# Kernel optimization log

Hardware: AMD Instinct MI355X
Metric: run time of the kernel (lower is better)

## Reference

```python
import jax, jax.numpy as jnp
import numpy as np

NUM_HEADS = 16
HEAD_DIM = 80
HIDDEN = 1280
SEQ = 3072
NUM_SEGS = 6  # 6 packed images of 512 patches each


def rotate_half(x):
    x1, x2 = jnp.split(x, 2, axis=-1)
    return jnp.concatenate([-x2, x1], axis=-1)


def setup_inputs() -> dict:
    key = jax.random.key(0)
    ks = jax.random.split(key, 6)
    hidden_states = jax.random.normal(ks[0], (SEQ, HIDDEN), dtype=jnp.float32)
    # RoPE tables as in Qwen-VL vision: freqs over half the head_dim, duplicated
    half = HEAD_DIM // 2
    inv_freq = 1.0 / (10000.0 ** (jnp.arange(half, dtype=jnp.float32) / half))
    pos = jnp.arange(SEQ, dtype=jnp.float32)[:, None]
    freqs = pos * inv_freq[None, :]                      # (SEQ, half)
    emb = jnp.concatenate([freqs, freqs], axis=-1)       # (SEQ, HEAD_DIM)
    cos = jnp.cos(emb)
    sin = jnp.sin(emb)
    # Packed segment boundaries: [0, 512, 1024, ..., 3072]
    cu_seqlens = jnp.arange(0, SEQ + 1, SEQ // NUM_SEGS, dtype=jnp.int32)
    scale = 0.02
    w_qkv = jax.random.normal(ks[1], (3 * HIDDEN, HIDDEN), dtype=jnp.float32) * scale
    b_qkv = jax.random.normal(ks[2], (3 * HIDDEN,), dtype=jnp.float32) * scale
    w_proj = jax.random.normal(ks[3], (HIDDEN, HIDDEN), dtype=jnp.float32) * scale
    b_proj = jax.random.normal(ks[4], (HIDDEN,), dtype=jnp.float32) * scale
    return {
        "hidden_states": hidden_states, "cos": cos, "sin": sin,
        "w_qkv": w_qkv, "b_qkv": b_qkv, "w_proj": w_proj, "b_proj": b_proj,
        "cu_seqlens": cu_seqlens,
    }


def reference(hidden_states, cos, sin, w_qkv, b_qkv, w_proj, b_proj, cu_seqlens):
    S, H = hidden_states.shape
    nh, hd = NUM_HEADS, H // NUM_HEADS

    # Fused QKV projection: (S, 3H) -> q, k, v each (S, nh, hd)
    qkv = hidden_states @ w_qkv.T + b_qkv
    qkv = qkv.reshape(S, 3, nh, hd)
    q, k, v = qkv[:, 0], qkv[:, 1], qkv[:, 2]

    # Inline RoPE on q/k (cos/sin broadcast over heads)
    c = cos[:, None, :]
    s = sin[:, None, :]
    q = q * c + rotate_half(q) * s
    k = k * c + rotate_half(k) * s

    # Original casts fp32 -> fp16 for the flash attention kernel
    q16 = q.astype(jnp.float16)
    k16 = k.astype(jnp.float16)
    v16 = v.astype(jnp.float16)

    # Varlen masking: tokens attend only within their own packed segment
    tok = jnp.arange(S)
    seg = jnp.searchsorted(cu_seqlens, tok, side="right")  # (S,)
    same_seg = seg[:, None] == seg[None, :]                 # (S, S)

    scale = hd ** (-0.5)
    # Scores accumulated in fp32 (as flash attention does internally)
    scores = jnp.einsum("qhd,khd->hqk", q16, k16,
                        preferred_element_type=jnp.float32) * scale
    scores = jnp.where(same_seg[None], scores, jnp.finfo(jnp.float32).min)
    weights = jax.nn.softmax(scores, axis=-1).astype(jnp.float16)  # (nh, S, S)

    attn = jnp.einsum("hqk,khd->qhd", weights, v16)  # (S, nh, hd) fp16
    attn = attn.astype(jnp.float32).reshape(S, H)
    return attn @ w_proj.T + b_proj
```

## Files before the change

### kernel.cpp

```cpp
#include <hip/hip_runtime.h>

typedef _Float16 f16;
typedef _Float16 half8 __attribute__((ext_vector_type(8)));
typedef _Float16 half4 __attribute__((ext_vector_type(4)));
typedef float f32x4 __attribute__((ext_vector_type(4)));

__device__ __forceinline__ void gld_lds16(const void* g, void* l) {
  __builtin_amdgcn_global_load_lds((const __attribute__((address_space(1))) void*)g,
                                   (__attribute__((address_space(3))) void*)l, 16, 0, 0);
}

template <int CTRL>
__device__ __forceinline__ float dppf(float x) {
  return __builtin_bit_cast(float,
      __builtin_amdgcn_mov_dpp(__builtin_bit_cast(int, x), CTRL, 0xf, 0xf, true));
}
__device__ __forceinline__ float dpp_max16(float v) {
  v = fmaxf(v, dppf<0xB1>(v));
  v = fmaxf(v, dppf<0x4E>(v));
  v = fmaxf(v, dppf<0x128>(v));
  v = fmaxf(v, dppf<0x140>(v));
  return v;
}
__device__ __forceinline__ float dpp_sum16(float v) {
  v += dppf<0xB1>(v);
  v += dppf<0x4E>(v);
  v += dppf<0x128>(v);
  v += dppf<0x140>(v);
  return v;
}

__global__ void cvt_all(const float* __restrict__ hid, const float* __restrict__ wq,
                        const float* __restrict__ wp, f16* __restrict__ hid16,
                        f16* __restrict__ wq16, f16* __restrict__ wp16) {
  int b = blockIdx.x;
  const float* in;
  f16* out;
  int i;
  if (b < 3840) { in = hid; out = hid16; i = b * 256 + threadIdx.x; }
  else if (b < 8640) { in = wq; out = wq16; i = (b - 3840) * 256 + threadIdx.x; }
  else { in = wp; out = wp16; i = (b - 8640) * 256 + threadIdx.x; }
  float4 v = ((const float4*)in)[i];
  half4 o;
  o.x = (f16)v.x; o.y = (f16)v.y; o.z = (f16)v.z; o.w = (f16)v.w;
  ((half4*)out)[i] = o;
}

__global__ __launch_bounds__(256, 2) void gemm240(const f16* __restrict__ A,
                                                  const f16* __restrict__ B,
                                                  const float* __restrict__ bias,
                                                  f16* __restrict__ C) {
  __shared__ f16 S[40960];
  char* Sb = (char*)S;
  const int tid = threadIdx.x, lane = tid & 63, wid = tid >> 6;
  const int lm = lane & 15, q4 = lane >> 4;
  const int wm = wid >> 1, wn = wid & 1;
  const int swz = ((int)blockIdx.x & 7) * 60 + ((int)blockIdx.x >> 3);
  const int bm = (swz % 24) * 128, bn = (swz / 24) * 192;

  const int ch = ((lane & 7) ^ (lane >> 3)) << 3;
  uint32_t aoff[4], boff[6];
#pragma unroll
  for (int j = 0; j < 4; j++)
    aoff[j] = (uint32_t)((bm + (j * 4 + wid) * 8 + (lane >> 3)) * 1280 + ch);
#pragma unroll
  for (int i = 0; i < 6; i++)
    boff[i] = (uint32_t)((bn + wid * 48 + i * 8 + (lane >> 3)) * 1280 + ch);

  const int xr = (lm & 7) << 4;
  int aro[4][2], bro[6][2];
#pragma unroll
  for (int f = 0; f < 4; f++)
#pragma unroll
    for (int ks = 0; ks < 2; ks++)
      aro[f][ks] = (wm * 64 + f * 16 + lm) * 128 + ((ks * 64 + q4 * 16) ^ xr);
#pragma unroll
  for (int n = 0; n < 6; n++)
#pragma unroll
    for (int ks = 0; ks < 2; ks++)
      bro[n][ks] = (wn * 96 + n * 16 + lm) * 128 + ((ks * 64 + q4 * 16) ^ xr);

  f32x4 acc[4][6] = {};

  {
#pragma unroll
    for (int j = 0; j < 4; j++)
      gld_lds16(A + aoff[j], Sb + (j * 4 + wid) * 1024);
#pragma unroll
    for (int i = 0; i < 6; i++)
      gld_lds16(B + boff[i], Sb + 32768 + (wid * 6 + i) * 1024);
    gld_lds16(A + aoff[0] + 64, Sb + 16384 + wid * 1024);
    gld_lds16(A + aoff[2] + 64, Sb + 16384 + (8 + wid) * 1024);
#pragma unroll
    for (int i = 0; i < 6; i++)
      gld_lds16(B + boff[i] + 64, Sb + 32768 + 24576 + (wid * 6 + i) * 1024);
    asm volatile("s_waitcnt vmcnt(8)" ::: "memory");
    __builtin_amdgcn_s_barrier();
  }

  constexpr int NT = 20;
  for (int t = 0; t < NT; ++t) {
    const int p = t & 1;
    char* Ab = Sb + p * 16384;
    char* Bb = Sb + 32768 + p * 24576;
    char* An = Sb + (p ^ 1) * 16384;
    const int k1 = (t + 1) * 64, k2 = (t + 2) * 64;

    half8 a0[2][2], bf[6][2];
#pragma unroll
    for (int f = 0; f < 2; f++)
#pragma unroll
      for (int ks = 0; ks < 2; ks++)
        a0[f][ks] = *(const half8*)(Ab + aro[f][ks]);
#pragma unroll
    for (int n = 0; n < 6; n++)
#pragma unroll
      for (int ks = 0; ks < 2; ks++)
        bf[n][ks] = *(const half8*)(Bb + bro[n][ks]);
    if (t + 1 < NT) {
      gld_lds16(A + aoff[1] + k1, An + (4 + wid) * 1024);
      gld_lds16(A + aoff[3] + k1, An + (12 + wid) * 1024);
    }
    __builtin_amdgcn_s_setprio(1);
#pragma unroll
    for (int ks = 0; ks < 2; ks++)
#pragma unroll
      for (int f = 0; f < 2; f++)
#pragma unroll
        for (int n = 0; n < 6; n++)
          acc[f][n] =
              __builtin_amdgcn_mfma_f32_16x16x32_f16(a0[f][ks], bf[n][ks], acc[f][n], 0, 0, 0);
    __builtin_amdgcn_s_setprio(0);
    __builtin_amdgcn_sched_barrier(0);
    asm volatile("s_waitcnt lgkmcnt(0)" ::: "memory");
    __builtin_amdgcn_s_barrier();

#pragma unroll
    for (int f = 0; f < 2; f++)
#pragma unroll
      for (int ks = 0; ks < 2; ks++)
        a0[f][ks] = *(const half8*)(Ab + aro[2 + f][ks]);
    if (t + 2 < NT) {
      gld_lds16(A + aoff[0] + k2, Ab + wid * 1024);
      gld_lds16(A + aoff[2] + k2, Ab + (8 + wid) * 1024);
#pragma unroll
      for (int i = 0; i < 6; i++)
        gld_lds16(B + boff[i] + k2, Bb + (wid * 6 + i) * 1024);
    }
    __builtin_amdgcn_s_setprio(1);
#pragma unroll
    for (int ks = 0; ks < 2; ks++)
#pragma unroll
      for (int f = 0; f < 2; f++)
#pragma unroll
        for (int n = 0; n < 6; n++)
          acc[2 + f][n] = __builtin_amdgcn_mfma_f32_16x16x32_f16(a0[f][ks], bf[n][ks],
                                                                 acc[2 + f][n], 0, 0, 0);
    __builtin_amdgcn_s_setprio(0);
    __builtin_amdgcn_sched_barrier(0);
    if (t + 2 < NT) {
      asm volatile("s_waitcnt vmcnt(8)" ::: "memory");
    } else {
      asm volatile("s_waitcnt vmcnt(0)" ::: "memory");
    }
    asm volatile("s_waitcnt lgkmcnt(0)" ::: "memory");
    __builtin_amdgcn_s_barrier();
  }

#pragma unroll
  for (int f = 0; f < 4; f++)
#pragma unroll
    for (int n = 0; n < 6; n++) {
      const int gc = bn + wn * 96 + n * 16 + lm;
      const float bb = bias[gc];
      const int gr0 = bm + wm * 64 + f * 16 + q4 * 4;
#pragma unroll
      for (int r = 0; r < 4; r++)
        C[(size_t)(gr0 + r) * 3840 + gc] = (f16)(acc[f][n][r] + bb);
    }
}

template <bool OUT_F16>
__global__ __launch_bounds__(256, 2) void gemm_bt64(const f16* __restrict__ A,
                                                    const f16* __restrict__ B,
                                                    const float* __restrict__ bias,
                                                    void* __restrict__ Cout,
                                                    int K, int lda, int ldb, int ldc) {
  __shared__ f16 As[64 * 32];
  __shared__ f16 Bs[128 * 32];
  const int tid = threadIdx.x, lane = tid & 63, wave = tid >> 6;
  const int bm = blockIdx.x * 64, bn = blockIdx.y * 128;
  const int wm = (wave & 1) * 32, wn = (wave >> 1) * 64;
  const int lm = lane & 15, kq = (lane >> 4) * 8;
  const int arow = tid >> 2, acol = (tid & 3) * 8;

  const f16* Ab = A + (size_t)(bm + arow) * lda + acol;
  const f16* Bb = B + (size_t)(bn + arow) * ldb + acol;
  f16* AsW = As + wave * 512;
  f16* BsW = Bs + wave * 512;

  f32x4 acc[2][4] = {};
  for (int k0 = 0; k0 < K; k0 += 32) {
    gld_lds16(Ab + k0, AsW);
    gld_lds16(Bb + k0, BsW);
    gld_lds16(Bb + (size_t)64 * ldb + k0, BsW + 2048);
    __syncthreads();
    half8 af[2], bf[4];
#pragma unroll
    for (int mt = 0; mt < 2; mt++) af[mt] = *(const half8*)&As[(wm + 16 * mt + lm) * 32 + kq];
#pragma unroll
    for (int nt = 0; nt < 4; nt++) bf[nt] = *(const half8*)&Bs[(wn + 16 * nt + lm) * 32 + kq];
#pragma unroll
    for (int mt = 0; mt < 2; mt++)
#pragma unroll
      for (int nt = 0; nt < 4; nt++)
        acc[mt][nt] = __builtin_amdgcn_mfma_f32_16x16x32_f16(af[mt], bf[nt], acc[mt][nt], 0, 0, 0);
    __syncthreads();
  }
  const int q4 = lane >> 4;
#pragma unroll
  for (int mt = 0; mt < 2; mt++)
#pragma unroll
    for (int nt = 0; nt < 4; nt++)
#pragma unroll
      for (int r = 0; r < 4; r++) {
        int gr = bm + wm + 16 * mt + 4 * q4 + r;
        int gc = bn + wn + 16 * nt + lm;
        float v = acc[mt][nt][r] + bias[gc];
        if (OUT_F16)
          ((f16*)Cout)[(size_t)gr * ldc + gc] = (f16)v;
        else
          ((float*)Cout)[(size_t)gr * ldc + gc] = v;
      }
}

__global__ void rope_transpose(f16* __restrict__ qkv, const float* __restrict__ cosb,
                               const float* __restrict__ sinb, f16* __restrict__ vt) {
  __shared__ f16 tile[64][72];
  const int b = blockIdx.x;
  if (b < 1920) {
    int idx = b * 256 + threadIdx.x;
    int c = idx % 5;
    int t = idx / 5;
    int h = t % 16; t /= 16;
    int qk = t & 1;
    int s = t >> 1;
    size_t base = (size_t)s * 3840 + qk * 1280 + h * 80 + c * 8;
    half8 x = *(half8*)&qkv[base];
    half8 y = *(half8*)&qkv[base + 40];
    const float* cp = cosb + s * 80 + c * 8;
    const float* sp = sinb + s * 80 + c * 8;
    half8 ox, oy;
#pragma unroll
    for (int i = 0; i < 8; i++) {
      float cs = cp[i], sn = sp[i];
      float xf = (float)x[i], yf = (float)y[i];
      ox[i] = (f16)(xf * cs - yf * sn);
      oy[i] = (f16)(yf * cs + xf * sn);
    }
    *(half8*)&qkv[base] = ox;
    *(half8*)&qkv[base + 40] = oy;
  } else {
    const int bb = b - 1920;
    const int bs = (bb % 48) * 64;
    const int bd = (bb / 48) * 64;
    const int r = threadIdx.x >> 2, c = (threadIdx.x & 3) * 16;
    *(uint4*)&tile[r][c] = *(const uint4*)&qkv[(size_t)(bs + r) * 3840 + 2560 + bd + c];
    *(uint4*)&tile[r][c + 8] = *(const uint4*)&qkv[(size_t)(bs + r) * 3840 + 2560 + bd + c + 8];
    __syncthreads();
    f16 tmp[16];
#pragma unroll
    for (int i = 0; i < 16; i++) tmp[i] = tile[c + i][r];
    *(uint4*)&vt[(size_t)(bd + r) * 3072 + bs + c] = *(uint4*)&tmp[0];
    *(uint4*)&vt[(size_t)(bd + r) * 3072 + bs + c + 8] = *(uint4*)&tmp[8];
  }
}

__global__ __launch_bounds__(256, 3) void flash_attn6(const f16* __restrict__ qkv,
                                                      const f16* __restrict__ vt,
                                                      f16* __restrict__ attn) {
  __shared__ f16 S[25088];
  const int tid = threadIdx.x, lane = tid & 63, wave = tid >> 6;
  const int lm = lane & 15, q4 = lane >> 4;
  const int h = blockIdx.x, g = blockIdx.z;
  const int qbase = g * 512 + blockIdx.y * 64 + wave * 16;
  f16* P = S + 20480 + wave * 1152;
  const half8 hz = {};

  const f16* qrow = qkv + (size_t)(qbase + lm) * 3840 + h * 80;
  half8 qf[3];
  qf[0] = *(const half8*)(qrow + q4 * 8);
  qf[1] = *(const half8*)(qrow + 32 + q4 * 8);
  qf[2] = (q4 < 2) ? *(const half8*)(qrow + 64 + q4 * 8) : hz;

  const bool isK = wave < 2;
  const f16* gsrc = isK ? qkv : vt;
  const uint32_t gstep = isK ? (uint32_t)(64 * 3840) : 64u;
  const int cbase = (wave & 1) * 5;
  const uint32_t ldsoff = (isK ? 0u : 5120u) + (uint32_t)cbase * 512u;
  uint32_t goff[5];
#pragma unroll
  for (int i = 0; i < 5; i++) {
    int t = (cbase + i) * 1024 + lane * 16;
    if (isK) {
      int row = t / 160, colb = t % 160;
      goff[i] = (uint32_t)((g * 512 + row) * 3840 + 1280 + h * 80 + (colb >> 1));
    } else {
      int vd = t >> 7, vsb = t & 127;
      int vsrc = vsb ^ ((vd & 7) << 4);
      goff[i] = (uint32_t)((h * 80 + vd) * 3072 + g * 512 + (vsrc >> 1));
    }
  }

  f32x4 oacc[5] = {};
  float mprev[4] = {-1e30f, -1e30f, -1e30f, -1e30f};
  float lsum[4] = {0.f, 0.f, 0.f, 0.f};
  const float sc = 0.11180339887498949f * 1.4426950408889634f;

#pragma unroll
  for (int i = 0; i < 5; i++) gld_lds16(gsrc + goff[i], S + ldsoff + i * 512);
  __syncthreads();

  for (int jj = 0; jj < 8; jj++) {
    const int p = jj & 1;
    f16* Kb = S + p * 10240;
    f16* Vb = Kb + 5120;
    if (jj < 7) {
#pragma unroll
      for (int i = 0; i < 5; i++)
        gld_lds16(gsrc + goff[i] + (uint32_t)(jj + 1) * gstep,
                  S + (p ^ 1) * 10240 + ldsoff + i * 512);
    }

    f32x4 sacc[4] = {};
#pragma unroll
    for (int ks = 0; ks < 3; ks++) {
      half8 bk[4];
#pragma unroll
      for (int nt = 0; nt < 4; nt++)
        bk[nt] = (ks < 2 || q4 < 2)
                     ? *(const half8*)&Kb[(16 * nt + lm) * 80 + 32 * ks + q4 * 8]
                     : hz;
#pragma unroll
      for (int nt = 0; nt < 4; nt++)
        sacc[nt] = __builtin_amdgcn_mfma_f32_16x16x32_f16(qf[ks], bk[nt], sacc[nt], 0, 0, 0);
    }

    float mnew[4], alpha[4], rs[4];
#pragma unroll
    for (int r = 0; r < 4; r++) {
      float v = fmaxf(fmaxf(sacc[0][r], sacc[1][r]), fmaxf(sacc[2][r], sacc[3][r]));
      v = dpp_max16(v);
      mnew[r] = fmaxf(mprev[r], v * sc);
      alpha[r] = __builtin_exp2f(mprev[r] - mnew[r]);
      mprev[r] = mnew[r];
      rs[r] = 0.f;
    }
#pragma unroll
    for (int nt = 0; nt < 4; nt++)
#pragma unroll
      for (int r = 0; r < 4; r++) {
        float pp = __builtin_exp2f(sacc[nt][r] * sc - mnew[r]);
        sacc[nt][r] = pp;
        rs[r] += pp;
      }
#pragma unroll
    for (int r = 0; r < 4; r++) {
      float v = dpp_sum16(rs[r]);
      lsum[r] = alpha[r] * lsum[r] + v;
#pragma unroll
      for (int nt2 = 0; nt2 < 5; nt2++) oacc[nt2][r] *= alpha[r];
    }

#pragma unroll
    for (int nt = 0; nt < 4; nt++)
#pragma unroll
      for (int r = 0; r < 4; r++)
        P[(4 * q4 + r) * 72 + 16 * nt + lm] = (f16)sacc[nt][r];

#pragma unroll
    for (int ks = 0; ks < 2; ks++) {
      half8 ap = *(const half8*)&P[lm * 72 + ks * 32 + q4 * 8];
      half8 bv[5];
#pragma unroll
      for (int nt2 = 0; nt2 < 5; nt2++) {
        int row = 16 * nt2 + lm;
        bv[nt2] = *(const half8*)&Vb[row * 64 + ((ks * 32 + q4 * 8) ^ ((row & 7) << 3))];
      }
#pragma unroll
      for (int nt2 = 0; nt2 < 5; nt2++)
        oacc[nt2] = __builtin_amdgcn_mfma_f32_16x16x32_f16(ap, bv[nt2], oacc[nt2], 0, 0, 0);
    }

    __syncthreads();
  }

#pragma unroll
  for (int r = 0; r < 4; r++) {
    float inv = 1.0f / lsum[r];
    int s = qbase + 4 * q4 + r;
#pragma unroll
    for (int nt2 = 0; nt2 < 5; nt2++)
      attn[(size_t)s * 1280 + h * 80 + 16 * nt2 + lm] = (f16)(oacc[nt2][r] * inv);
  }
}

extern "C" void kernel_launch(void* const* d_in, const int* in_sizes, int n_in,
                              void* d_out, int out_size, void* d_ws, size_t ws_size,
                              hipStream_t stream) {
  const float* hidden = (const float*)d_in[0];
  const float* cosb   = (const float*)d_in[1];
  const float* sinb   = (const float*)d_in[2];
  const float* w_qkv  = (const float*)d_in[3];
  const float* b_qkv  = (const float*)d_in[4];
  const float* w_proj = (const float*)d_in[5];
  const float* b_proj = (const float*)d_in[6];

  char* ws = (char*)d_ws;
  f16* hidden16 = (f16*)(ws + 0);
  f16* wqkv16   = (f16*)(ws + 7864320);
  f16* wproj16  = (f16*)(ws + 17694720);
  f16* qkv16    = (f16*)(ws + 20971520);
  f16* attn16   = (f16*)(ws + 44564480);
  f16* vt16     = hidden16;

  cvt_all<<<10240, 256, 0, stream>>>(hidden, w_qkv, w_proj, hidden16, wqkv16, wproj16);

  gemm240<<<480, 256, 0, stream>>>(hidden16, wqkv16, b_qkv, qkv16);

  rope_transpose<<<2880, 256, 0, stream>>>(qkv16, cosb, sinb, vt16);

  flash_attn6<<<dim3(16, 8, 6), 256, 0, stream>>>(qkv16, vt16, attn16);

  gemm_bt64<false><<<dim3(48, 10), 256, 0, stream>>>(attn16, wproj16, b_proj, d_out,
                                                     1280, 1280, 1280, 1280);
}
```

Baseline: 186.0 us.

## Replace output projection GEMM with double-buffered swizzled LDS pipelined kernel

```diff
diff --git a/kernel.cpp b/kernel.cpp
--- a/kernel.cpp
+++ b/kernel.cpp
@@ -65,7 +65,7 @@
     aoff[j] = (uint32_t)((bm + (j * 4 + wid) * 8 + (lane >> 3)) * 1280 + ch);
 #pragma unroll
   for (int i = 0; i < 6; i++)
-    boff[i] = (uint32_t)((bn + wid * 48 + i * 8 + (lane >> 3)) * 1280 + ch);
+    boff[i] = (uint32_t)((bn + (wid * 6 + i) * 8 + (lane >> 3)) * 1280 + ch);
 
   const int xr = (lm & 7) << 4;
   int aro[4][2], bro[6][2];
@@ -180,58 +180,123 @@
     }
 }
 
-template <bool OUT_F16>
-__global__ __launch_bounds__(256, 2) void gemm_bt64(const f16* __restrict__ A,
+__global__ __launch_bounds__(256, 2) void gemm_proj(const f16* __restrict__ A,
                                                     const f16* __restrict__ B,
                                                     const float* __restrict__ bias,
-                                                    void* __restrict__ Cout,
-                                                    int K, int lda, int ldb, int ldc) {
-  __shared__ f16 As[64 * 32];
-  __shared__ f16 Bs[128 * 32];
-  const int tid = threadIdx.x, lane = tid & 63, wave = tid >> 6;
+                                                    float* __restrict__ C) {
+  __shared__ f16 S[24576];
+  char* Sb = (char*)S;
+  const int tid = threadIdx.x, lane = tid & 63, wid = tid >> 6;
+  const int lm = lane & 15, q4 = lane >> 4;
+  const int wm = wid >> 1, wn = wid & 1;
   const int bm = blockIdx.x * 64, bn = blockIdx.y * 128;
-  const int wm = (wave & 1) * 32, wn = (wave >> 1) * 64;
-  const int lm = lane & 15, kq = (lane >> 4) * 8;
-  const int arow = tid >> 2, acol = (tid & 3) * 8;
-
-  const f16* Ab = A + (size_t)(bm + arow) * lda + acol;
-  const f16* Bb = B + (size_t)(bn + arow) * ldb + acol;
-  f16* AsW = As + wave * 512;
-  f16* BsW = Bs + wave * 512;
+
+  const int ch = ((lane & 7) ^ (lane >> 3)) << 3;
+  const int cH1 = (wid & 1) + (wid >> 1) * 4;
+  const int cH2 = cH1 + 2;
+  const uint32_t aoffH1 = (uint32_t)((bm + cH1 * 8 + (lane >> 3)) * 1280 + ch);
+  const uint32_t aoffH2 = (uint32_t)((bm + cH2 * 8 + (lane >> 3)) * 1280 + ch);
+  uint32_t boff[4];
+#pragma unroll
+  for (int i = 0; i < 4; i++)
+    boff[i] = (uint32_t)((bn + (wid * 4 + i) * 8 + (lane >> 3)) * 1280 + ch);
+
+  const int xr = (lm & 7) << 4;
+  int aro[2][2], bro[4][2];
+#pragma unroll
+  for (int f = 0; f < 2; f++)
+#pragma unroll
+    for (int ks = 0; ks < 2; ks++)
+      aro[f][ks] = (wm * 32 + f * 16 + lm) * 128 + ((ks * 64 + q4 * 16) ^ xr);
+#pragma unroll
+  for (int n = 0; n < 4; n++)
+#pragma unroll
+    for (int ks = 0; ks < 2; ks++)
+      bro[n][ks] = (wn * 64 + n * 16 + lm) * 128 + ((ks * 64 + q4 * 16) ^ xr);
 
   f32x4 acc[2][4] = {};
-  for (int k0 = 0; k0 < K; k0 += 32) {
-    gld_lds16(Ab + k0, AsW);
-    gld_lds16(Bb + k0, BsW);
-    gld_lds16(Bb + (size_t)64 * ldb + k0, BsW + 2048);
-    __syncthreads();
-    half8 af[2], bf[4];
-#pragma unroll
-    for (int mt = 0; mt < 2; mt++) af[mt] = *(const half8*)&As[(wm + 16 * mt + lm) * 32 + kq];
-#pragma unroll
-    for (int nt = 0; nt < 4; nt++) bf[nt] = *(const half8*)&Bs[(wn + 16 * nt + lm) * 32 + kq];
-#pragma unroll
-    for (int mt = 0; mt < 2; mt++)
-#pragma unroll
-      for (int nt = 0; nt < 4; nt++)
-        acc[mt][nt] = __builtin_amdgcn_mfma_f32_16x16x32_f16(af[mt], bf[nt], acc[mt][nt], 0, 0, 0);
-    __syncthreads();
-  }
-  const int q4 = lane >> 4;
-#pragma unroll
-  for (int mt = 0; mt < 2; mt++)
-#pragma unroll
-    for (int nt = 0; nt < 4; nt++)
-#pragma unroll
-      for (int r = 0; r < 4; r++) {
-        int gr = bm + wm + 16 * mt + 4 * q4 + r;
-        int gc = bn + wn + 16 * nt + lm;
-        float v = acc[mt][nt][r] + bias[gc];
-        if (OUT_F16)
-          ((f16*)Cout)[(size_t)gr * ldc + gc] = (f16)v;
-        else
-          ((float*)Cout)[(size_t)gr * ldc + gc] = v;
-      }
+
+  {
+    gld_lds16(A + aoffH1, Sb + cH1 * 1024);
+    gld_lds16(A + aoffH2, Sb + cH2 * 1024);
+#pragma unroll
+    for (int i = 0; i < 4; i++)
+      gld_lds16(B + boff[i], Sb + 16384 + (wid * 4 + i) * 1024);
+    gld_lds16(A + aoffH1 + 64, Sb + 8192 + cH1 * 1024);
+#pragma unroll
+    for (int i = 0; i < 4; i++)
+      gld_lds16(B + boff[i] + 64, Sb + 32768 + (wid * 4 + i) * 1024);
+    asm volatile("s_waitcnt vmcnt(5)" ::: "memory");
+    __builtin_amdgcn_s_barrier();
+  }
+
+  constexpr int NT = 20;
+  for (int t = 0; t < NT; ++t) {
+    const int p = t & 1;
+    char* Ab = Sb + p * 8192;
+    char* Bb = Sb + 16384 + p * 16384;
+    char* An = Sb + (p ^ 1) * 8192;
+    const int k1 = (t + 1) * 64, k2 = (t + 2) * 64;
+
+    half8 a0[2], bf[4][2];
+#pragma unroll
+    for (int ks = 0; ks < 2; ks++)
+      a0[ks] = *(const half8*)(Ab + aro[0][ks]);
+#pragma unroll
+    for (int n = 0; n < 4; n++)
+#pragma unroll
+      for (int ks = 0; ks < 2; ks++)
+        bf[n][ks] = *(const half8*)(Bb + bro[n][ks]);
+    if (t + 1 < NT)
+      gld_lds16(A + aoffH2 + k1, An + cH2 * 1024);
+    __builtin_amdgcn_s_setprio(1);
+#pragma unroll
+    for (int ks = 0; ks < 2; ks++)
+#pragma unroll
+      for (int n = 0; n < 4; n++)
+        acc[0][n] = __builtin_amdgcn_mfma_f32_16x16x32_f16(a0[ks], bf[n][ks], acc[0][n], 0, 0, 0);
+    __builtin_amdgcn_s_setprio(0);
+    __builtin_amdgcn_sched_barrier(0);
+    asm volatile("s_waitcnt lgkmcnt(0)" ::: "memory");
+    __builtin_amdgcn_s_barrier();
+
+#pragma unroll
+    for (int ks = 0; ks < 2; ks++)
+      a0[ks] = *(const half8*)(Ab + aro[1][ks]);
+    if (t + 2 < NT) {
+      gld_lds16(A + aoffH1 + k2, Ab + cH1 * 1024);
+#pragma unroll
+      for (int i = 0; i < 4; i++)
+        gld_lds16(B + boff[i] + k2, Bb + (wid * 4 + i) * 1024);
+    }
+    __builtin_amdgcn_s_setprio(1);
+#pragma unroll
+    for (int ks = 0; ks < 2; ks++)
+#pragma unroll
+      for (int n = 0; n < 4; n++)
+        acc[1][n] = __builtin_amdgcn_mfma_f32_16x16x32_f16(a0[ks], bf[n][ks], acc[1][n], 0, 0, 0);
+    __builtin_amdgcn_s_setprio(0);
+    __builtin_amdgcn_sched_barrier(0);
+    if (t + 2 < NT) {
+      asm volatile("s_waitcnt vmcnt(5)" ::: "memory");
+    } else {
+      asm volatile("s_waitcnt vmcnt(0)" ::: "memory");
+    }
+    asm volatile("s_waitcnt lgkmcnt(0)" ::: "memory");
+    __builtin_amdgcn_s_barrier();
+  }
+
+#pragma unroll
+  for (int f = 0; f < 2; f++)
+#pragma unroll
+    for (int n = 0; n < 4; n++) {
+      const int gc = bn + wn * 64 + n * 16 + lm;
+      const float bb = bias[gc];
+      const int gr0 = bm + wm * 32 + f * 16 + q4 * 4;
+#pragma unroll
+      for (int r = 0; r < 4; r++)
+        C[(size_t)(gr0 + r) * 1280 + gc] = acc[f][n][r] + bb;
+    }
 }
 
 __global__ void rope_transpose(f16* __restrict__ qkv, const float* __restrict__ cosb,
@@ -432,6 +497,5 @@
 
   flash_attn6<<<dim3(16, 8, 6), 256, 0, stream>>>(qkv16, vt16, attn16);
 
-  gemm_bt64<false><<<dim3(48, 10), 256, 0, stream>>>(attn16, wproj16, b_proj, d_out,
-                                                     1280, 1280, 1280, 1280);
-}
+  gemm_proj<<<dim3(48, 10), 256, 0, stream>>>(attn16, wproj16, b_proj, (float*)d_out);
+}
```

Measured after the change: 184.3 us. No clear change (-1.0%).
